# Optimization experiments

Hardware: AMD Instinct MI355X
Metric: run time of the kernel (lower is better)

## Reference

```python
import jax, jax.numpy as jnp
import numpy as np

B, S, H = 4, 4096, 2048
E = 64          # num_routed_experts
TOP_K = 8
TEMP = 1.0      # router_temperature


def setup_inputs() -> dict:
    key = jax.random.key(0)
    k1, k2 = jax.random.split(key)
    hidden_states = jax.random.normal(k1, (B, S, H), dtype=jnp.float32)
    # nn.Linear weight: [out_features, in_features] = [E, H]
    gate_w = jax.random.normal(k2, (E, H), dtype=jnp.float32) * (1.0 / np.sqrt(H))
    return {"hidden_states": hidden_states, "gate_w": gate_w}


def reference(hidden_states, gate_w):
    # Gate projection + temperature scaling: [B,S,H] @ [H,E] -> [B,S,E]
    router_logits = jnp.einsum("bsh,eh->bse", hidden_states, gate_w) / TEMP
    # Top-k over experts
    routing_weights, selected_experts = jax.lax.top_k(router_logits, TOP_K)
    # Softmax over the top-k slots in fp32, cast back to input dtype
    routing_weights = jax.nn.softmax(routing_weights.astype(jnp.float32), axis=-1).astype(hidden_states.dtype)
    return router_logits, routing_weights, selected_experts
```

## Files before the change

kernel.cpp:

```cpp
#include <hip/hip_runtime.h>
#include <math.h>

#define HH 2048
#define EE 64
#define TOPK 8
#define NT 16384
#define MT 32
#define KC 128
#define NCH 16
#define LS 68

typedef __attribute__((ext_vector_type(8)))  short short8;
typedef __attribute__((ext_vector_type(16))) float f32x16;

static __device__ __forceinline__ void cvt3(const float4& a, const float4& b,
                                            short8& h, short8& m, short8& l)
{
    const float v[8] = {a.x, a.y, a.z, a.w, b.x, b.y, b.z, b.w};
#pragma unroll
    for (int i = 0; i < 8; ++i) {
        const unsigned int u = __float_as_uint(v[i]);
        h[i] = (short)(u >> 16);
        const float r1 = v[i] - __uint_as_float(u & 0xffff0000u);
        const unsigned int u1 = __float_as_uint(r1);
        m[i] = (short)(u1 >> 16);
        const float r2 = r1 - __uint_as_float(u1 & 0xffff0000u);
        const unsigned int u2 = __float_as_uint(r2);
        l[i] = (short)((u2 + 0x7fffu + ((u2 >> 16) & 1u)) >> 16);
    }
}

__global__ __launch_bounds__(256) void wsplit(
    const float* __restrict__ w, short* __restrict__ wsw)
{
    const int e = blockIdx.x;
    const int o = threadIdx.x;
    const int k = o * 8;
    const float4 a = *(const float4*)(w + (size_t)e * HH + k);
    const float4 b = *(const float4*)(w + (size_t)e * HH + k + 4);
    short8 h, m, l;
    cvt3(a, b, h, m, l);

    const int eb  = e >> 5, lr = e & 31;
    const int s16 = o >> 1;
    const int l5  = o & 1;
    const int lane = l5 * 32 + lr;
    short* dst = wsw + (((size_t)(eb * 128 + s16) * 3) * 64 + lane) * 8;
    *(short8*)(dst)           = h;
    *(short8*)(dst + 64 * 8)  = m;
    *(short8*)(dst + 128 * 8) = l;
}

__global__ __launch_bounds__(512, 4) void router_fused(
    const float* __restrict__ x,
    const short* __restrict__ wsw,
    float* __restrict__ out_logits,
    float* __restrict__ out_wts,
    float* __restrict__ out_idx)
{
    __shared__ __align__(16) short8 xsl[2][1536];
    float* slog = (float*)xsl;

    const int t    = threadIdx.x;
    const int wv   = t >> 6;
    const int lane = t & 63;
    const int eb   = wv & 1;
    const int kq   = wv >> 1;
    const int l5   = lane >> 5;
    const int lr   = lane & 31;
    const int tok0 = blockIdx.x * MT;

    const int sr = t >> 4;
    const int su = t & 15;
    const float* xg = x + (size_t)(tok0 + sr) * HH + su * 8;
    const int s16s = su >> 1;
    const int lfs  = (su & 1) * 32 + sr;

    f32x16 accM = {0}, accS = {0};
    float4 xr0, xr1;

    auto sload = [&](int c) {
        xr0 = *(const float4*)(xg + (size_t)c * KC);
        xr1 = *(const float4*)(xg + (size_t)c * KC + 4);
    };
    auto swrite = [&](int buf) {
        short8 h, m, l;
        cvt3(xr0, xr1, h, m, l);
        const int b0 = s16s * 3;
        xsl[buf][((b0 + 0) << 6) + (lfs ^ ((b0 + 0) & 7))] = h;
        xsl[buf][((b0 + 1) << 6) + (lfs ^ ((b0 + 1) & 7))] = m;
        xsl[buf][((b0 + 2) << 6) + (lfs ^ ((b0 + 2) & 7))] = l;
    };
    auto chunk = [&](int c, int buf) {
#pragma unroll
        for (int st = 0; st < 2; ++st) {
            const int s16l = kq * 2 + st;
            const int s16g = c * 8 + s16l;
            const short8* wp = (const short8*)wsw
                             + ((size_t)(eb * 128 + s16g) * 3) * 64 + lane;
            const short8 B0 = wp[0];
            const short8 B1 = wp[64];
            const short8 B2 = wp[128];
            const int ab = s16l * 3;
            const short8 Ah = xsl[buf][((ab + 0) << 6) + (lane ^ ((ab + 0) & 7))];
            const short8 Am = xsl[buf][((ab + 1) << 6) + (lane ^ ((ab + 1) & 7))];
            const short8 Al = xsl[buf][((ab + 2) << 6) + (lane ^ ((ab + 2) & 7))];
            accM = __builtin_amdgcn_mfma_f32_32x32x16_bf16(Ah, B0, accM, 0, 0, 0);
            accS = __builtin_amdgcn_mfma_f32_32x32x16_bf16(Ah, B1, accS, 0, 0, 0);
            accS = __builtin_amdgcn_mfma_f32_32x32x16_bf16(Am, B0, accS, 0, 0, 0);
            accS = __builtin_amdgcn_mfma_f32_32x32x16_bf16(Ah, B2, accS, 0, 0, 0);
            accS = __builtin_amdgcn_mfma_f32_32x32x16_bf16(Al, B0, accS, 0, 0, 0);
            accS = __builtin_amdgcn_mfma_f32_32x32x16_bf16(Am, B1, accS, 0, 0, 0);
        }
    };

    sload(0);
    swrite(0);
    __syncthreads();

#pragma unroll 1
    for (int c = 0; c < NCH; ++c) {
        if (c + 1 < NCH) sload(c + 1);
        chunk(c, c & 1);
        if (c + 1 < NCH) swrite((c + 1) & 1);
        __syncthreads();
    }

    const int col = eb * 32 + lr;
#pragma unroll 1
    for (int q = 0; q < 4; ++q) {
        if (kq == q) {
#pragma unroll
            for (int r = 0; r < 16; ++r) {
                const int row = (r & 3) + 8 * (r >> 2) + 4 * l5;
                const float val = accM[r] + accS[r];
                if (q == 0) slog[row * LS + col] = val;
                else        slog[row * LS + col] += val;
            }
        }
        __syncthreads();
    }

    {
        const int row = t >> 4;
        const int c4  = (t & 15) * 4;
        const float4 o0 = *(const float4*)&slog[row * LS + c4];
        *(float4*)(out_logits + (size_t)(tok0 + row) * EE + c4) = o0;
    }

    if (t < MT) {
        float tv[TOPK];
        int   ti[TOPK];
#pragma unroll
        for (int q = 0; q < TOPK; ++q) { tv[q] = -INFINITY; ti[q] = 0; }

        for (int e = 0; e < EE; ++e) {
            const float val = slog[t * LS + e];
            if (val > tv[TOPK - 1]) {
                tv[TOPK - 1] = val;
                ti[TOPK - 1] = e;
#pragma unroll
                for (int q = TOPK - 1; q > 0; --q) {
                    if (tv[q] > tv[q - 1]) {
                        float fv = tv[q]; tv[q] = tv[q - 1]; tv[q - 1] = fv;
                        int   fi = ti[q]; ti[q] = ti[q - 1]; ti[q - 1] = fi;
                    }
                }
            }
        }

        const float m = tv[0];
        float ew[TOPK];
        float sum = 0.f;
#pragma unroll
        for (int q = 0; q < TOPK; ++q) { ew[q] = expf(tv[q] - m); sum += ew[q]; }
        const float inv = 1.f / sum;

        const size_t tok = (size_t)(tok0 + t);
        float4 w0, w1, i0, i1;
        w0.x = ew[0] * inv; w0.y = ew[1] * inv; w0.z = ew[2] * inv; w0.w = ew[3] * inv;
        w1.x = ew[4] * inv; w1.y = ew[5] * inv; w1.z = ew[6] * inv; w1.w = ew[7] * inv;
        i0.x = (float)ti[0]; i0.y = (float)ti[1]; i0.z = (float)ti[2]; i0.w = (float)ti[3];
        i1.x = (float)ti[4]; i1.y = (float)ti[5]; i1.z = (float)ti[6]; i1.w = (float)ti[7];
        *(float4*)(out_wts + tok * TOPK)     = w0;
        *(float4*)(out_wts + tok * TOPK + 4) = w1;
        *(float4*)(out_idx + tok * TOPK)     = i0;
        *(float4*)(out_idx + tok * TOPK + 4) = i1;
    }
}

extern "C" void kernel_launch(void* const* d_in, const int* in_sizes, int n_in,
                              void* d_out, int out_size, void* d_ws, size_t ws_size,
                              hipStream_t stream) {
    const float* x = (const float*)d_in[0];
    const float* w = (const float*)d_in[1];
    float* out        = (float*)d_out;
    float* out_logits = out;
    float* out_wts    = out + (size_t)NT * EE;
    float* out_idx    = out_wts + (size_t)NT * TOPK;
    short* wsw = (short*)d_ws;

    hipLaunchKernelGGL(wsplit, dim3(EE), dim3(256), 0, stream, w, wsw);
    hipLaunchKernelGGL(router_fused, dim3(NT / MT), dim3(512), 0, stream,
                       x, wsw, out_logits, out_wts, out_idx);
}
```

Before: 219.8 us.

## Double token tile per block to 64 with 1024-thread blocks and halved K chunk

```diff
diff --git a/kernel.cpp b/kernel.cpp
--- a/kernel.cpp
+++ b/kernel.cpp
@@ -5,9 +5,9 @@
 #define EE 64
 #define TOPK 8
 #define NT 16384
-#define MT 32
-#define KC 128
-#define NCH 16
+#define MT 64
+#define KC 64
+#define NCH 32
 #define LS 68
 
 typedef __attribute__((ext_vector_type(8)))  short short8;
@@ -51,7 +51,7 @@
     *(short8*)(dst + 128 * 8) = l;
 }
 
-__global__ __launch_bounds__(512, 4) void router_fused(
+__global__ __launch_bounds__(1024, 4) void router_fused(
     const float* __restrict__ x,
     const short* __restrict__ wsw,
     float* __restrict__ out_logits,
@@ -65,16 +65,18 @@
     const int wv   = t >> 6;
     const int lane = t & 63;
     const int eb   = wv & 1;
-    const int kq   = wv >> 1;
+    const int kq   = (wv >> 1) & 3;
+    const int tg   = wv >> 3;
     const int l5   = lane >> 5;
     const int lr   = lane & 31;
     const int tok0 = blockIdx.x * MT;
 
-    const int sr = t >> 4;
-    const int su = t & 15;
+    const int sr  = t >> 3;
+    const int su  = t & 7;
     const float* xg = x + (size_t)(tok0 + sr) * HH + su * 8;
     const int s16s = su >> 1;
-    const int lfs  = (su & 1) * 32 + sr;
+    const int tgs  = sr >> 5;
+    const int lfs  = (su & 1) * 32 + (sr & 31);
 
     f32x16 accM = {0}, accS = {0};
     float4 xr0, xr1;
@@ -86,43 +88,42 @@
     auto swrite = [&](int buf) {
         short8 h, m, l;
         cvt3(xr0, xr1, h, m, l);
-        const int b0 = s16s * 3;
-        xsl[buf][((b0 + 0) << 6) + (lfs ^ ((b0 + 0) & 7))] = h;
-        xsl[buf][((b0 + 1) << 6) + (lfs ^ ((b0 + 1) & 7))] = m;
-        xsl[buf][((b0 + 2) << 6) + (lfs ^ ((b0 + 2) & 7))] = l;
+        const int b0 = (s16s * 3 + 0) * 2 + tgs;
+        const int b1 = (s16s * 3 + 1) * 2 + tgs;
+        const int b2 = (s16s * 3 + 2) * 2 + tgs;
+        xsl[buf][(b0 << 6) + (lfs ^ (b0 & 7))] = h;
+        xsl[buf][(b1 << 6) + (lfs ^ (b1 & 7))] = m;
+        xsl[buf][(b2 << 6) + (lfs ^ (b2 & 7))] = l;
     };
     auto chunk = [&](int c, int buf) {
-#pragma unroll
-        for (int st = 0; st < 2; ++st) {
-            const int s16l = kq * 2 + st;
-            const int s16g = c * 8 + s16l;
-            const short8* wp = (const short8*)wsw
-                             + ((size_t)(eb * 128 + s16g) * 3) * 64 + lane;
-            const short8 B0 = wp[0];
-            const short8 B1 = wp[64];
-            const short8 B2 = wp[128];
-            const int ab = s16l * 3;
-            const short8 Ah = xsl[buf][((ab + 0) << 6) + (lane ^ ((ab + 0) & 7))];
-            const short8 Am = xsl[buf][((ab + 1) << 6) + (lane ^ ((ab + 1) & 7))];
-            const short8 Al = xsl[buf][((ab + 2) << 6) + (lane ^ ((ab + 2) & 7))];
-            accM = __builtin_amdgcn_mfma_f32_32x32x16_bf16(Ah, B0, accM, 0, 0, 0);
-            accS = __builtin_amdgcn_mfma_f32_32x32x16_bf16(Ah, B1, accS, 0, 0, 0);
-            accS = __builtin_amdgcn_mfma_f32_32x32x16_bf16(Am, B0, accS, 0, 0, 0);
-            accS = __builtin_amdgcn_mfma_f32_32x32x16_bf16(Ah, B2, accS, 0, 0, 0);
-            accS = __builtin_amdgcn_mfma_f32_32x32x16_bf16(Al, B0, accS, 0, 0, 0);
-            accS = __builtin_amdgcn_mfma_f32_32x32x16_bf16(Am, B1, accS, 0, 0, 0);
-        }
+        const int s16g = c * 4 + kq;
+        const short8* wp = (const short8*)wsw
+                         + ((size_t)(eb * 128 + s16g) * 3) * 64 + lane;
+        const short8 B0 = wp[0];
+        const short8 B1 = wp[64];
+        const short8 B2 = wp[128];
+        const int a0 = (kq * 3 + 0) * 2 + tg;
+        const int a1 = (kq * 3 + 1) * 2 + tg;
+        const int a2 = (kq * 3 + 2) * 2 + tg;
+        const short8 Ah = xsl[buf][(a0 << 6) + (lane ^ (a0 & 7))];
+        const short8 Am = xsl[buf][(a1 << 6) + (lane ^ (a1 & 7))];
+        const short8 Al = xsl[buf][(a2 << 6) + (lane ^ (a2 & 7))];
+        accM = __builtin_amdgcn_mfma_f32_32x32x16_bf16(Ah, B0, accM, 0, 0, 0);
+        accS = __builtin_amdgcn_mfma_f32_32x32x16_bf16(Ah, B1, accS, 0, 0, 0);
+        accS = __builtin_amdgcn_mfma_f32_32x32x16_bf16(Am, B0, accS, 0, 0, 0);
+        accS = __builtin_amdgcn_mfma_f32_32x32x16_bf16(Ah, B2, accS, 0, 0, 0);
+        accS = __builtin_amdgcn_mfma_f32_32x32x16_bf16(Al, B0, accS, 0, 0, 0);
+        accS = __builtin_amdgcn_mfma_f32_32x32x16_bf16(Am, B1, accS, 0, 0, 0);
     };
 
-    sload(0);
-    swrite(0);
+    if (t < 512) { sload(0); swrite(0); }
     __syncthreads();
 
 #pragma unroll 1
     for (int c = 0; c < NCH; ++c) {
-        if (c + 1 < NCH) sload(c + 1);
+        if (t < 512 && c + 1 < NCH) sload(c + 1);
         chunk(c, c & 1);
-        if (c + 1 < NCH) swrite((c + 1) & 1);
+        if (t < 512 && c + 1 < NCH) swrite((c + 1) & 1);
         __syncthreads();
     }
 
@@ -132,7 +133,7 @@
         if (kq == q) {
 #pragma unroll
             for (int r = 0; r < 16; ++r) {
-                const int row = (r & 3) + 8 * (r >> 2) + 4 * l5;
+                const int row = tg * 32 + (r & 3) + 8 * (r >> 2) + 4 * l5;
                 const float val = accM[r] + accS[r];
                 if (q == 0) slog[row * LS + col] = val;
                 else        slog[row * LS + col] += val;
@@ -201,6 +202,6 @@
     short* wsw = (short*)d_ws;
 
     hipLaunchKernelGGL(wsplit, dim3(EE), dim3(256), 0, stream, w, wsw);
-    hipLaunchKernelGGL(router_fused, dim3(NT / MT), dim3(512), 0, stream,
+    hipLaunchKernelGGL(router_fused, dim3(NT / MT), dim3(1024), 0, stream,
                        x, wsw, out_logits, out_wts, out_idx);
 }
```

Measured after the change: 222.5 us. No clear change (+1.2%).

## Stage fp32 activations directly into LDS and split to bf16 at consumption

Applied to the files above, without the earlier changes.

```diff
diff --git a/kernel.cpp b/kernel.cpp
--- a/kernel.cpp
+++ b/kernel.cpp
@@ -12,6 +12,9 @@
 
 typedef __attribute__((ext_vector_type(8)))  short short8;
 typedef __attribute__((ext_vector_type(16))) float f32x16;
+
+#define GLB(p) ((const __attribute__((address_space(1))) void*)(p))
+#define LDS(p) ((__attribute__((address_space(3))) void*)(p))
 
 static __device__ __forceinline__ void cvt3(const float4& a, const float4& b,
                                             short8& h, short8& m, short8& l)
@@ -58,8 +61,8 @@
     float* __restrict__ out_wts,
     float* __restrict__ out_idx)
 {
-    __shared__ __align__(16) short8 xsl[2][1536];
-    float* slog = (float*)xsl;
+    __shared__ __align__(16) float xtile[2][MT * KC];
+    float* slog = (float*)xtile;
 
     const int t    = threadIdx.x;
     const int wv   = t >> 6;
@@ -70,41 +73,40 @@
     const int lr   = lane & 31;
     const int tok0 = blockIdx.x * MT;
 
-    const int sr = t >> 4;
-    const int su = t & 15;
-    const float* xg = x + (size_t)(tok0 + sr) * HH + su * 8;
-    const int s16s = su >> 1;
-    const int lfs  = (su & 1) * 32 + sr;
+    const int r0 = t >> 5;
+    const int u0s = t & 31;
+    const int wbase = (t & ~63) * 4;
 
     f32x16 accM = {0}, accS = {0};
-    float4 xr0, xr1;
-
-    auto sload = [&](int c) {
-        xr0 = *(const float4*)(xg + (size_t)c * KC);
-        xr1 = *(const float4*)(xg + (size_t)c * KC + 4);
+
+    auto stage = [&](int c, int buf) {
+#pragma unroll
+        for (int j = 0; j < 2; ++j) {
+            const int r = r0 + j * 16;
+            const size_t goff = (size_t)(tok0 + r) * HH + c * KC
+                              + ((u0s ^ (r & 7)) << 2);
+            float* lp = &xtile[buf][wbase + j * 2048];
+            __builtin_amdgcn_global_load_lds(GLB(x + goff), LDS(lp), 16, 0, 0);
+        }
     };
-    auto swrite = [&](int buf) {
-        short8 h, m, l;
-        cvt3(xr0, xr1, h, m, l);
-        const int b0 = s16s * 3;
-        xsl[buf][((b0 + 0) << 6) + (lfs ^ ((b0 + 0) & 7))] = h;
-        xsl[buf][((b0 + 1) << 6) + (lfs ^ ((b0 + 1) & 7))] = m;
-        xsl[buf][((b0 + 2) << 6) + (lfs ^ ((b0 + 2) & 7))] = l;
-    };
+
     auto chunk = [&](int c, int buf) {
 #pragma unroll
         for (int st = 0; st < 2; ++st) {
-            const int s16l = kq * 2 + st;
-            const int s16g = c * 8 + s16l;
+            const int s    = kq * 2 + st;
+            const int s16g = c * 8 + s;
             const short8* wp = (const short8*)wsw
                              + ((size_t)(eb * 128 + s16g) * 3) * 64 + lane;
             const short8 B0 = wp[0];
             const short8 B1 = wp[64];
             const short8 B2 = wp[128];
-            const int ab = s16l * 3;
-            const short8 Ah = xsl[buf][((ab + 0) << 6) + (lane ^ ((ab + 0) & 7))];
-            const short8 Am = xsl[buf][((ab + 1) << 6) + (lane ^ ((ab + 1) & 7))];
-            const short8 Al = xsl[buf][((ab + 2) << 6) + (lane ^ ((ab + 2) & 7))];
+            const int v0 = s * 4 + l5 * 2;
+            const float4 f0 = *(const float4*)
+                &xtile[buf][lr * KC + ((v0      ^ (lr & 7)) << 2)];
+            const float4 f1 = *(const float4*)
+                &xtile[buf][lr * KC + (((v0 + 1) ^ (lr & 7)) << 2)];
+            short8 Ah, Am, Al;
+            cvt3(f0, f1, Ah, Am, Al);
             accM = __builtin_amdgcn_mfma_f32_32x32x16_bf16(Ah, B0, accM, 0, 0, 0);
             accS = __builtin_amdgcn_mfma_f32_32x32x16_bf16(Ah, B1, accS, 0, 0, 0);
             accS = __builtin_amdgcn_mfma_f32_32x32x16_bf16(Am, B0, accS, 0, 0, 0);
@@ -114,15 +116,13 @@
         }
     };
 
-    sload(0);
-    swrite(0);
+    stage(0, 0);
     __syncthreads();
 
 #pragma unroll 1
     for (int c = 0; c < NCH; ++c) {
-        if (c + 1 < NCH) sload(c + 1);
+        if (c + 1 < NCH) stage(c + 1, (c + 1) & 1);
         chunk(c, c & 1);
-        if (c + 1 < NCH) swrite((c + 1) & 1);
         __syncthreads();
     }
 
```

Result: faster. 215.3 us (-2.1%).
